# Optimization experiments

Measured on AMD Instinct MI355X. Metric: run time of the kernel, lower is better.

## Reference

```python
import jax, jax.numpy as jnp
import numpy as np

B, S, H, F, E, TOPK = 4, 2048, 1024, 3584, 8, 2
W_SCALE = 0.02  # keep router logits / activations numerically sane


def setup_inputs() -> dict:
    key = jax.random.key(0)
    k1, k2, k3, k4, k5 = jax.random.split(key, 5)
    return {
        "hidden_states": jax.random.normal(k1, (B, S, H), dtype=jnp.float32),
        "gate_w": jax.random.normal(k2, (E, H), dtype=jnp.float32) * W_SCALE,
        "w1": jax.random.normal(k3, (E, F, H), dtype=jnp.float32) * W_SCALE,
        "w2": jax.random.normal(k4, (E, H, F), dtype=jnp.float32) * W_SCALE,
        "w3": jax.random.normal(k5, (E, F, H), dtype=jnp.float32) * W_SCALE,
        "top_k": TOPK,
    }


def reference(hidden_states, gate_w, w1, w2, w3, top_k):
    b, s, h = hidden_states.shape
    x = hidden_states.reshape(-1, h)                       # [T, H]
    router_logits = x @ gate_w.T                           # [T, E]
    probs = jax.nn.softmax(router_logits.astype(jnp.float32), axis=-1)
    routing_weights, selected_experts = jax.lax.top_k(probs, top_k)  # [T, k]
    routing_weights = routing_weights / routing_weights.sum(axis=-1, keepdims=True)
    routing_weights = routing_weights.astype(x.dtype)
    n_experts = gate_w.shape[0]
    # combine weights: [T, E], zero for unselected experts
    combine = (jax.nn.one_hot(selected_experts, n_experts, dtype=routing_weights.dtype)
               * routing_weights[..., None]).sum(axis=1)
    out = jnp.zeros_like(x)
    for e in range(n_experts):
        hgate = jax.nn.silu(x @ w1[e].T) * (x @ w3[e].T)   # [T, F]
        out = out + (hgate @ w2[e].T) * combine[:, e:e + 1]
    return out.reshape(b, s, h), router_logits
```

## Files before the change

kernel.cpp:

```cpp
#include <hip/hip_runtime.h>
#include <hip/hip_bf16.h>
#include <stdint.h>

#define T_TOK 8192
#define H_DIM 1024
#define F_DIM 3584
#define E_NUM 8

#define BM 128
#define BN 128
#define BK 32
#define LDT 40

typedef __attribute__((ext_vector_type(8))) short bf16x8;
typedef __attribute__((ext_vector_type(4))) float f32x4;

__device__ __forceinline__ short f2bf(float f) {
    union { float f; uint32_t u; } v; v.f = f;
    uint32_t r = v.u + 0x7fffu + ((v.u >> 16) & 1u);
    return (short)(r >> 16);
}

__device__ __forceinline__ uint32_t pack_bf16x2(float a, float b) {
    union { float f; uint32_t u; } ua, ub;
    ua.f = a; ub.f = b;
    return __builtin_amdgcn_perm(ub.u + 0x8000u, ua.u + 0x8000u, 0x07060302u);
}

__device__ __forceinline__ void cvt_store16(const f32x4* v, short* dst) {
    uint32_t w[8];
    #pragma unroll
    for (int i = 0; i < 4; i++) {
        w[2*i]   = pack_bf16x2(v[i][0], v[i][1]);
        w[2*i+1] = pack_bf16x2(v[i][2], v[i][3]);
    }
    ((uint32_t*)dst)[0] = w[0]; ((uint32_t*)dst)[1] = w[1];
    ((uint32_t*)dst)[2] = w[2]; ((uint32_t*)dst)[3] = w[3];
    ((uint32_t*)dst)[4] = w[4]; ((uint32_t*)dst)[5] = w[5];
    ((uint32_t*)dst)[6] = w[6]; ((uint32_t*)dst)[7] = w[7];
}

__device__ __forceinline__ void zero16_store(short* dst) {
    bf16x8 z;
    #pragma unroll
    for (int i = 0; i < 8; i++) z[i] = 0;
    *(bf16x8*)dst = z;
    *((bf16x8*)dst + 1) = z;
}

__device__ __forceinline__ void load16(f32x4* dst, const float* __restrict__ src) {
    const f32x4* p = (const f32x4*)src;
    #pragma unroll
    for (int i = 0; i < 4; i++) dst[i] = p[i];
}

__global__ void router_kernel(const float* __restrict__ x,
                              const float* __restrict__ gate_w,
                              float* __restrict__ logits_out,
                              int* __restrict__ counts,
                              int* __restrict__ lists,
                              float* __restrict__ wgt) {
    int wave = (blockIdx.x * blockDim.x + threadIdx.x) >> 6;
    int lane = threadIdx.x & 63;
    if (wave >= T_TOK) return;
    const float* xr = x + (size_t)wave * H_DIM;

    float acc[E_NUM];
    #pragma unroll
    for (int e = 0; e < E_NUM; e++) acc[e] = 0.f;

    for (int i = lane; i < H_DIM; i += 64) {
        float xv = xr[i];
        #pragma unroll
        for (int e = 0; e < E_NUM; e++) acc[e] += xv * gate_w[e * H_DIM + i];
    }
    #pragma unroll
    for (int off = 32; off > 0; off >>= 1) {
        #pragma unroll
        for (int e = 0; e < E_NUM; e++) acc[e] += __shfl_xor(acc[e], off);
    }

    if (lane == 0) {
        int t = wave;
        #pragma unroll
        for (int e = 0; e < E_NUM; e++) logits_out[t * E_NUM + e] = acc[e];
        int i0 = 0; float v0 = acc[0];
        #pragma unroll
        for (int e = 1; e < E_NUM; e++) if (acc[e] > v0) { v0 = acc[e]; i0 = e; }
        int i1 = -1; float v1 = -1e30f;
        #pragma unroll
        for (int e = 0; e < E_NUM; e++) if (e != i0 && acc[e] > v1) { v1 = acc[e]; i1 = e; }
        float e1 = __expf(v1 - v0);
        float inv = 1.f / (1.f + e1);
        int a0 = 2 * t, a1 = 2 * t + 1;
        wgt[a0] = inv;
        wgt[a1] = e1 * inv;
        int p0 = atomicAdd(&counts[i0], 1);
        lists[i0 * T_TOK + p0] = a0;
        int p1 = atomicAdd(&counts[i1], 1);
        lists[i1 * T_TOK + p1] = a1;
    }
}

__global__ __launch_bounds__(256, 2)
void gemm1_kernel(const float* __restrict__ x,
                  const float* __restrict__ w1,
                  const float* __restrict__ w3,
                  const int* __restrict__ counts,
                  const int* __restrict__ lists,
                  unsigned short* __restrict__ hgate) {
    const int e = blockIdx.z;
    const int count = counts[e];
    const int mbase = blockIdx.y * BM;
    if (mbase >= count) return;
    const int nbase = blockIdx.x * BN;

    __shared__ short As[BM * LDT];
    __shared__ short B1s[BN * LDT];
    __shared__ short B3s[BN * LDT];

    const int tid = threadIdx.x;
    const int r = tid >> 1;
    const int half = tid & 1;

    const float* arow = nullptr;
    {
        int m = mbase + r;
        if (m < count) {
            int a = lists[e * T_TOK + m];
            arow = x + (size_t)(a >> 1) * H_DIM;
        }
    }
    const float* b1row = w1 + ((size_t)e * F_DIM + (nbase + r)) * H_DIM;
    const float* b3row = w3 + ((size_t)e * F_DIM + (nbase + r)) * H_DIM;

    const int lane = tid & 63;
    const int wid = tid >> 6;
    const int wm = wid >> 1, wn = wid & 1;
    const int lr = lane & 15, lq = lane >> 4;

    f32x4 acc1[4][4], acc3[4][4];
    #pragma unroll
    for (int i = 0; i < 4; i++)
        #pragma unroll
        for (int j = 0; j < 4; j++) {
            acc1[i][j] = (f32x4){0.f, 0.f, 0.f, 0.f};
            acc3[i][j] = (f32x4){0.f, 0.f, 0.f, 0.f};
        }

    f32x4 ap[4], b1p[4], b3p[4];
    {
        const int koff = half * 16;
        if (arow) load16(ap, arow + koff);
        load16(b1p, b1row + koff);
        load16(b3p, b3row + koff);
    }

    short* adst  = &As[r * LDT + half * 16];
    short* b1dst = &B1s[r * LDT + half * 16];
    short* b3dst = &B3s[r * LDT + half * 16];

    for (int k0 = 0; k0 < H_DIM; k0 += BK) {
        if (arow) cvt_store16(ap, adst); else zero16_store(adst);
        cvt_store16(b1p, b1dst);
        cvt_store16(b3p, b3dst);
        __syncthreads();

        int kn = k0 + BK;
        if (kn < H_DIM) {
            const int koff = kn + half * 16;
            if (arow) load16(ap, arow + koff);
            load16(b1p, b1row + koff);
            load16(b3p, b3row + koff);
        }

        bf16x8 af[4], b1f[4], b3f[4];
        #pragma unroll
        for (int i = 0; i < 4; i++)
            af[i] = *(const bf16x8*)&As[(wm * 64 + i * 16 + lr) * LDT + lq * 8];
        #pragma unroll
        for (int j = 0; j < 4; j++) {
            b1f[j] = *(const bf16x8*)&B1s[(wn * 64 + j * 16 + lr) * LDT + lq * 8];
            b3f[j] = *(const bf16x8*)&B3s[(wn * 64 + j * 16 + lr) * LDT + lq * 8];
        }
        #pragma unroll
        for (int i = 0; i < 4; i++)
            #pragma unroll
            for (int j = 0; j < 4; j++) {
                acc1[i][j] = __builtin_amdgcn_mfma_f32_16x16x32_bf16(af[i], b1f[j], acc1[i][j], 0, 0, 0);
                acc3[i][j] = __builtin_amdgcn_mfma_f32_16x16x32_bf16(af[i], b3f[j], acc3[i][j], 0, 0, 0);
            }
        __syncthreads();
    }

    #pragma unroll
    for (int i = 0; i < 4; i++) {
        #pragma unroll
        for (int rg = 0; rg < 4; rg++) {
            int mm = mbase + wm * 64 + i * 16 + lq * 4 + rg;
            if (mm >= count) continue;
            int a = lists[e * T_TOK + mm];
            unsigned short* hrow = hgate + (size_t)a * F_DIM + nbase;
            #pragma unroll
            for (int j = 0; j < 4; j++) {
                float g = acc1[i][j][rg];
                float u = acc3[i][j][rg];
                float s = (g / (1.f + __expf(-g))) * u;
                hrow[wn * 64 + j * 16 + lr] = (unsigned short)f2bf(s);
            }
        }
    }
}

__global__ __launch_bounds__(256, 2)
void gemm2_kernel(const unsigned short* __restrict__ hgate,
                  const float* __restrict__ w2,
                  const int* __restrict__ counts,
                  const int* __restrict__ lists,
                  const float* __restrict__ wgt,
                  float* __restrict__ out) {
    const int e = blockIdx.z;
    const int count = counts[e];
    const int mbase = blockIdx.y * BM;
    if (mbase >= count) return;
    const int nbase = blockIdx.x * BN;

    __shared__ short As[BM * LDT];
    __shared__ short Bs[BN * LDT];

    const int tid = threadIdx.x;
    const int r = tid >> 1;
    const int half = tid & 1;

    const unsigned short* arow = nullptr;
    {
        int m = mbase + r;
        if (m < count) {
            int a = lists[e * T_TOK + m];
            arow = hgate + (size_t)a * F_DIM;
        }
    }
    const float* brow = w2 + ((size_t)e * H_DIM + (nbase + r)) * F_DIM;

    const int lane = tid & 63;
    const int wid = tid >> 6;
    const int wm = wid >> 1, wn = wid & 1;
    const int lr = lane & 15, lq = lane >> 4;

    f32x4 acc[4][4];
    #pragma unroll
    for (int i = 0; i < 4; i++)
        #pragma unroll
        for (int j = 0; j < 4; j++) acc[i][j] = (f32x4){0.f, 0.f, 0.f, 0.f};

    bf16x8 a2p[2];
    f32x4 bp[4];
    {
        const int koff = half * 16;
        if (arow) {
            const bf16x8* p = (const bf16x8*)(arow + koff);
            a2p[0] = p[0]; a2p[1] = p[1];
        }
        load16(bp, brow + koff);
    }

    short* adst = &As[r * LDT + half * 16];
    short* bdst = &Bs[r * LDT + half * 16];

    for (int k0 = 0; k0 < F_DIM; k0 += BK) {
        if (arow) {
            *(bf16x8*)adst = a2p[0];
            *((bf16x8*)adst + 1) = a2p[1];
        } else {
            zero16_store(adst);
        }
        cvt_store16(bp, bdst);
        __syncthreads();

        int kn = k0 + BK;
        if (kn < F_DIM) {
            const int koff = kn + half * 16;
            if (arow) {
                const bf16x8* p = (const bf16x8*)(arow + koff);
                a2p[0] = p[0]; a2p[1] = p[1];
            }
            load16(bp, brow + koff);
        }

        bf16x8 af[4], bf[4];
        #pragma unroll
        for (int i = 0; i < 4; i++)
            af[i] = *(const bf16x8*)&As[(wm * 64 + i * 16 + lr) * LDT + lq * 8];
        #pragma unroll
        for (int j = 0; j < 4; j++)
            bf[j] = *(const bf16x8*)&Bs[(wn * 64 + j * 16 + lr) * LDT + lq * 8];
        #pragma unroll
        for (int i = 0; i < 4; i++)
            #pragma unroll
            for (int j = 0; j < 4; j++)
                acc[i][j] = __builtin_amdgcn_mfma_f32_16x16x32_bf16(af[i], bf[j], acc[i][j], 0, 0, 0);
        __syncthreads();
    }

    #pragma unroll
    for (int i = 0; i < 4; i++) {
        #pragma unroll
        for (int rg = 0; rg < 4; rg++) {
            int mm = mbase + wm * 64 + i * 16 + lq * 4 + rg;
            if (mm >= count) continue;
            int a = lists[e * T_TOK + mm];
            float w = wgt[a];
            int t = a >> 1;
            float* orow = out + (size_t)t * H_DIM + nbase;
            #pragma unroll
            for (int j = 0; j < 4; j++)
                atomicAdd(&orow[wn * 64 + j * 16 + lr], acc[i][j][rg] * w);
        }
    }
}

extern "C" void kernel_launch(void* const* d_in, const int* in_sizes, int n_in,
                              void* d_out, int out_size, void* d_ws, size_t ws_size,
                              hipStream_t stream) {
    const float* x      = (const float*)d_in[0];
    const float* gate_w = (const float*)d_in[1];
    const float* w1     = (const float*)d_in[2];
    const float* w2     = (const float*)d_in[3];
    const float* w3     = (const float*)d_in[4];

    float* out    = (float*)d_out;
    float* logits = out + (size_t)T_TOK * H_DIM;

    char* ws = (char*)d_ws;
    int*   counts = (int*)(ws + 0);
    int*   lists  = (int*)(ws + 1024);
    float* wgt    = (float*)(ws + 1024 + (size_t)E_NUM * T_TOK * 4);
    unsigned short* hgate =
        (unsigned short*)(ws + 1024 + (size_t)E_NUM * T_TOK * 4 + (size_t)T_TOK * 2 * 4);

    hipMemsetAsync(counts, 0, E_NUM * sizeof(int), stream);
    hipMemsetAsync(out, 0, (size_t)T_TOK * H_DIM * sizeof(float), stream);

    router_kernel<<<T_TOK / 4, 256, 0, stream>>>(x, gate_w, logits, counts, lists, wgt);

    gemm1_kernel<<<dim3(F_DIM / BN, T_TOK / BM, E_NUM), 256, 0, stream>>>(
        x, w1, w3, counts, lists, hgate);

    gemm2_kernel<<<dim3(H_DIM / BN, T_TOK / BM, E_NUM), 256, 0, stream>>>(
        hgate, w2, counts, lists, wgt, out);
}
```

Measured before the change: 1.227 ms.

## Pre-convert inputs to bf16 and stage GEMM tiles with direct global-to-LDS loads

```diff
diff --git a/kernel.cpp b/kernel.cpp
--- a/kernel.cpp
+++ b/kernel.cpp
@@ -14,6 +14,7 @@
 
 typedef __attribute__((ext_vector_type(8))) short bf16x8;
 typedef __attribute__((ext_vector_type(4))) float f32x4;
+typedef __attribute__((ext_vector_type(4))) unsigned int u32x4;
 
 __device__ __forceinline__ short f2bf(float f) {
     union { float f; uint32_t u; } v; v.f = f;
@@ -34,10 +35,8 @@
         w[2*i]   = pack_bf16x2(v[i][0], v[i][1]);
         w[2*i+1] = pack_bf16x2(v[i][2], v[i][3]);
     }
-    ((uint32_t*)dst)[0] = w[0]; ((uint32_t*)dst)[1] = w[1];
-    ((uint32_t*)dst)[2] = w[2]; ((uint32_t*)dst)[3] = w[3];
-    ((uint32_t*)dst)[4] = w[4]; ((uint32_t*)dst)[5] = w[5];
-    ((uint32_t*)dst)[6] = w[6]; ((uint32_t*)dst)[7] = w[7];
+    #pragma unroll
+    for (int i = 0; i < 8; i++) ((uint32_t*)dst)[i] = w[i];
 }
 
 __device__ __forceinline__ void zero16_store(short* dst) {
@@ -52,6 +51,13 @@
     const f32x4* p = (const f32x4*)src;
     #pragma unroll
     for (int i = 0; i < 4; i++) dst[i] = p[i];
+}
+
+__device__ __forceinline__ void gload16(const unsigned short* g, unsigned short* l) {
+    __builtin_amdgcn_global_load_lds(
+        (const __attribute__((address_space(1))) void*)g,
+        (__attribute__((address_space(3))) void*)l,
+        16, 0, 0);
 }
 
 __global__ void router_kernel(const float* __restrict__ x,
@@ -102,13 +108,218 @@
     }
 }
 
+__global__ void cvt_bf16_kernel(const float* __restrict__ in,
+                                unsigned short* __restrict__ out, int n8) {
+    int i = blockIdx.x * blockDim.x + threadIdx.x;
+    int stride = gridDim.x * blockDim.x;
+    for (; i < n8; i += stride) {
+        const f32x4* p = (const f32x4*)in + 2 * (size_t)i;
+        f32x4 v0 = p[0], v1 = p[1];
+        u32x4 w;
+        w[0] = pack_bf16x2(v0[0], v0[1]);
+        w[1] = pack_bf16x2(v0[2], v0[3]);
+        w[2] = pack_bf16x2(v1[0], v1[1]);
+        w[3] = pack_bf16x2(v1[2], v1[3]);
+        *(u32x4*)(out + 8 * (size_t)i) = w;
+    }
+}
+
 __global__ __launch_bounds__(256, 2)
-void gemm1_kernel(const float* __restrict__ x,
-                  const float* __restrict__ w1,
-                  const float* __restrict__ w3,
-                  const int* __restrict__ counts,
-                  const int* __restrict__ lists,
-                  unsigned short* __restrict__ hgate) {
+void gemm1_bf(const unsigned short* __restrict__ xbf,
+              const unsigned short* __restrict__ w1bf,
+              const unsigned short* __restrict__ w3bf,
+              const int* __restrict__ counts,
+              const int* __restrict__ lists,
+              const unsigned short* __restrict__ zbuf,
+              unsigned short* __restrict__ hgate) {
+    const int e = blockIdx.z;
+    const int count = counts[e];
+    const int mbase = blockIdx.x * BM;
+    if (mbase >= count) return;
+    const int nbase = blockIdx.y * BN;
+
+    __shared__ unsigned short As[BM * BK];
+    __shared__ unsigned short B1s[BN * BK];
+    __shared__ unsigned short B3s[BN * BK];
+
+    const int tid = threadIdx.x;
+    const int lane = tid & 63;
+    const int w = tid >> 6;
+    const int sr0 = w * 16 + (lane >> 2);
+    const int sr1 = 64 + sr0;
+    const int chunk = lane & 3;
+
+    const unsigned short* a0;
+    const unsigned short* a1;
+    {
+        int m = mbase + sr0;
+        a0 = (m < count) ? xbf + (size_t)(lists[e * T_TOK + m] >> 1) * H_DIM + chunk * 8
+                         : zbuf + chunk * 8;
+        m = mbase + sr1;
+        a1 = (m < count) ? xbf + (size_t)(lists[e * T_TOK + m] >> 1) * H_DIM + chunk * 8
+                         : zbuf + chunk * 8;
+    }
+    const unsigned short* b10 = w1bf + ((size_t)e * F_DIM + nbase + sr0) * H_DIM + chunk * 8;
+    const unsigned short* b11 = w1bf + ((size_t)e * F_DIM + nbase + sr1) * H_DIM + chunk * 8;
+    const unsigned short* b30 = w3bf + ((size_t)e * F_DIM + nbase + sr0) * H_DIM + chunk * 8;
+    const unsigned short* b31 = w3bf + ((size_t)e * F_DIM + nbase + sr1) * H_DIM + chunk * 8;
+
+    unsigned short* Al0  = &As[(size_t)(w * 16) * BK];
+    unsigned short* Al1  = &As[(size_t)(64 + w * 16) * BK];
+    unsigned short* B1l0 = &B1s[(size_t)(w * 16) * BK];
+    unsigned short* B1l1 = &B1s[(size_t)(64 + w * 16) * BK];
+    unsigned short* B3l0 = &B3s[(size_t)(w * 16) * BK];
+    unsigned short* B3l1 = &B3s[(size_t)(64 + w * 16) * BK];
+
+    const int wm = w >> 1, wn = w & 1;
+    const int lr = lane & 15, lq = lane >> 4;
+
+    f32x4 acc1[4][4], acc3[4][4];
+    #pragma unroll
+    for (int i = 0; i < 4; i++)
+        #pragma unroll
+        for (int j = 0; j < 4; j++) {
+            acc1[i][j] = (f32x4){0.f, 0.f, 0.f, 0.f};
+            acc3[i][j] = (f32x4){0.f, 0.f, 0.f, 0.f};
+        }
+
+    for (int k0 = 0; k0 < H_DIM; k0 += BK) {
+        gload16(a0, Al0);  gload16(a1, Al1);
+        gload16(b10, B1l0); gload16(b11, B1l1);
+        gload16(b30, B3l0); gload16(b31, B3l1);
+        a0 += BK; a1 += BK; b10 += BK; b11 += BK; b30 += BK; b31 += BK;
+        __syncthreads();
+
+        bf16x8 af[4];
+        #pragma unroll
+        for (int i = 0; i < 4; i++)
+            af[i] = *(const bf16x8*)&As[(wm * 64 + i * 16 + lr) * BK + lq * 8];
+        #pragma unroll
+        for (int j = 0; j < 4; j++) {
+            bf16x8 b1f = *(const bf16x8*)&B1s[(wn * 64 + j * 16 + lr) * BK + lq * 8];
+            bf16x8 b3f = *(const bf16x8*)&B3s[(wn * 64 + j * 16 + lr) * BK + lq * 8];
+            #pragma unroll
+            for (int i = 0; i < 4; i++) {
+                acc1[i][j] = __builtin_amdgcn_mfma_f32_16x16x32_bf16(af[i], b1f, acc1[i][j], 0, 0, 0);
+                acc3[i][j] = __builtin_amdgcn_mfma_f32_16x16x32_bf16(af[i], b3f, acc3[i][j], 0, 0, 0);
+            }
+        }
+        __syncthreads();
+    }
+
+    #pragma unroll
+    for (int i = 0; i < 4; i++) {
+        #pragma unroll
+        for (int rg = 0; rg < 4; rg++) {
+            int mm = mbase + wm * 64 + i * 16 + lq * 4 + rg;
+            if (mm >= count) continue;
+            int a = lists[e * T_TOK + mm];
+            unsigned short* hrow = hgate + (size_t)a * F_DIM + nbase;
+            #pragma unroll
+            for (int j = 0; j < 4; j++) {
+                float g = acc1[i][j][rg];
+                float u = acc3[i][j][rg];
+                float s = (g / (1.f + __expf(-g))) * u;
+                hrow[wn * 64 + j * 16 + lr] = (unsigned short)f2bf(s);
+            }
+        }
+    }
+}
+
+__global__ __launch_bounds__(256, 3)
+void gemm2_bf(const unsigned short* __restrict__ hgate,
+              const unsigned short* __restrict__ w2bf,
+              const int* __restrict__ counts,
+              const int* __restrict__ lists,
+              const float* __restrict__ wgt,
+              const unsigned short* __restrict__ zbuf,
+              float* __restrict__ out) {
+    const int e = blockIdx.z;
+    const int count = counts[e];
+    const int mbase = blockIdx.x * BM;
+    if (mbase >= count) return;
+    const int nbase = blockIdx.y * BN;
+
+    __shared__ unsigned short As[BM * BK];
+    __shared__ unsigned short Bs[BN * BK];
+
+    const int tid = threadIdx.x;
+    const int lane = tid & 63;
+    const int w = tid >> 6;
+    const int sr0 = w * 16 + (lane >> 2);
+    const int sr1 = 64 + sr0;
+    const int chunk = lane & 3;
+
+    const unsigned short* a0;
+    const unsigned short* a1;
+    {
+        int m = mbase + sr0;
+        a0 = (m < count) ? hgate + (size_t)lists[e * T_TOK + m] * F_DIM + chunk * 8
+                         : zbuf + chunk * 8;
+        m = mbase + sr1;
+        a1 = (m < count) ? hgate + (size_t)lists[e * T_TOK + m] * F_DIM + chunk * 8
+                         : zbuf + chunk * 8;
+    }
+    const unsigned short* b0 = w2bf + ((size_t)e * H_DIM + nbase + sr0) * F_DIM + chunk * 8;
+    const unsigned short* b1 = w2bf + ((size_t)e * H_DIM + nbase + sr1) * F_DIM + chunk * 8;
+
+    unsigned short* Al0 = &As[(size_t)(w * 16) * BK];
+    unsigned short* Al1 = &As[(size_t)(64 + w * 16) * BK];
+    unsigned short* Bl0 = &Bs[(size_t)(w * 16) * BK];
+    unsigned short* Bl1 = &Bs[(size_t)(64 + w * 16) * BK];
+
+    const int wm = w >> 1, wn = w & 1;
+    const int lr = lane & 15, lq = lane >> 4;
+
+    f32x4 acc[4][4];
+    #pragma unroll
+    for (int i = 0; i < 4; i++)
+        #pragma unroll
+        for (int j = 0; j < 4; j++) acc[i][j] = (f32x4){0.f, 0.f, 0.f, 0.f};
+
+    for (int k0 = 0; k0 < F_DIM; k0 += BK) {
+        gload16(a0, Al0); gload16(a1, Al1);
+        gload16(b0, Bl0); gload16(b1, Bl1);
+        a0 += BK; a1 += BK; b0 += BK; b1 += BK;
+        __syncthreads();
+
+        bf16x8 af[4];
+        #pragma unroll
+        for (int i = 0; i < 4; i++)
+            af[i] = *(const bf16x8*)&As[(wm * 64 + i * 16 + lr) * BK + lq * 8];
+        #pragma unroll
+        for (int j = 0; j < 4; j++) {
+            bf16x8 bf = *(const bf16x8*)&Bs[(wn * 64 + j * 16 + lr) * BK + lq * 8];
+            #pragma unroll
+            for (int i = 0; i < 4; i++)
+                acc[i][j] = __builtin_amdgcn_mfma_f32_16x16x32_bf16(af[i], bf, acc[i][j], 0, 0, 0);
+        }
+        __syncthreads();
+    }
+
+    #pragma unroll
+    for (int i = 0; i < 4; i++) {
+        #pragma unroll
+        for (int rg = 0; rg < 4; rg++) {
+            int mm = mbase + wm * 64 + i * 16 + lq * 4 + rg;
+            if (mm >= count) continue;
+            int a = lists[e * T_TOK + mm];
+            float wv = wgt[a];
+            float* orow = out + (size_t)(a >> 1) * H_DIM + nbase;
+            #pragma unroll
+            for (int j = 0; j < 4; j++)
+                atomicAdd(&orow[wn * 64 + j * 16 + lr], acc[i][j][rg] * wv);
+        }
+    }
+}
+
+__global__ __launch_bounds__(256, 2)
+void gemm1_f32(const float* __restrict__ x,
+               const float* __restrict__ w1,
+               const float* __restrict__ w3,
+               const int* __restrict__ counts,
+               const int* __restrict__ lists,
+               unsigned short* __restrict__ hgate) {
     const int e = blockIdx.z;
     const int count = counts[e];
     const int mbase = blockIdx.y * BM;
@@ -126,10 +337,7 @@
     const float* arow = nullptr;
     {
         int m = mbase + r;
-        if (m < count) {
-            int a = lists[e * T_TOK + m];
-            arow = x + (size_t)(a >> 1) * H_DIM;
-        }
+        if (m < count) arow = x + (size_t)(lists[e * T_TOK + m] >> 1) * H_DIM;
     }
     const float* b1row = w1 + ((size_t)e * F_DIM + (nbase + r)) * H_DIM;
     const float* b3row = w3 + ((size_t)e * F_DIM + (nbase + r)) * H_DIM;
@@ -155,7 +363,6 @@
         load16(b1p, b1row + koff);
         load16(b3p, b3row + koff);
     }
-
     short* adst  = &As[r * LDT + half * 16];
     short* b1dst = &B1s[r * LDT + half * 16];
     short* b3dst = &B3s[r * LDT + half * 16];
@@ -165,7 +372,6 @@
         cvt_store16(b1p, b1dst);
         cvt_store16(b3p, b3dst);
         __syncthreads();
-
         int kn = k0 + BK;
         if (kn < H_DIM) {
             const int koff = kn + half * 16;
@@ -173,26 +379,22 @@
             load16(b1p, b1row + koff);
             load16(b3p, b3row + koff);
         }
-
-        bf16x8 af[4], b1f[4], b3f[4];
+        bf16x8 af[4];
         #pragma unroll
         for (int i = 0; i < 4; i++)
             af[i] = *(const bf16x8*)&As[(wm * 64 + i * 16 + lr) * LDT + lq * 8];
         #pragma unroll
         for (int j = 0; j < 4; j++) {
-            b1f[j] = *(const bf16x8*)&B1s[(wn * 64 + j * 16 + lr) * LDT + lq * 8];
-            b3f[j] = *(const bf16x8*)&B3s[(wn * 64 + j * 16 + lr) * LDT + lq * 8];
-        }
-        #pragma unroll
-        for (int i = 0; i < 4; i++)
-            #pragma unroll
-            for (int j = 0; j < 4; j++) {
-                acc1[i][j] = __builtin_amdgcn_mfma_f32_16x16x32_bf16(af[i], b1f[j], acc1[i][j], 0, 0, 0);
-                acc3[i][j] = __builtin_amdgcn_mfma_f32_16x16x32_bf16(af[i], b3f[j], acc3[i][j], 0, 0, 0);
+            bf16x8 b1f = *(const bf16x8*)&B1s[(wn * 64 + j * 16 + lr) * LDT + lq * 8];
+            bf16x8 b3f = *(const bf16x8*)&B3s[(wn * 64 + j * 16 + lr) * LDT + lq * 8];
+            #pragma unroll
+            for (int i = 0; i < 4; i++) {
+                acc1[i][j] = __builtin_amdgcn_mfma_f32_16x16x32_bf16(af[i], b1f, acc1[i][j], 0, 0, 0);
+                acc3[i][j] = __builtin_amdgcn_mfma_f32_16x16x32_bf16(af[i], b3f, acc3[i][j], 0, 0, 0);
             }
-        __syncthreads();
-    }
-
+        }
+        __syncthreads();
+    }
     #pragma unroll
     for (int i = 0; i < 4; i++) {
         #pragma unroll
@@ -213,12 +415,12 @@
 }
 
 __global__ __launch_bounds__(256, 2)
-void gemm2_kernel(const unsigned short* __restrict__ hgate,
-                  const float* __restrict__ w2,
-                  const int* __restrict__ counts,
-                  const int* __restrict__ lists,
-                  const float* __restrict__ wgt,
-                  float* __restrict__ out) {
+void gemm2_f32(const unsigned short* __restrict__ hgate,
+               const float* __restrict__ w2,
+               const int* __restrict__ counts,
+               const int* __restrict__ lists,
+               const float* __restrict__ wgt,
+               float* __restrict__ out) {
     const int e = blockIdx.z;
     const int count = counts[e];
     const int mbase = blockIdx.y * BM;
@@ -235,10 +437,7 @@
     const unsigned short* arow = nullptr;
     {
         int m = mbase + r;
-        if (m < count) {
-            int a = lists[e * T_TOK + m];
-            arow = hgate + (size_t)a * F_DIM;
-        }
+        if (m < count) arow = hgate + (size_t)lists[e * T_TOK + m] * F_DIM;
     }
     const float* brow = w2 + ((size_t)e * H_DIM + (nbase + r)) * F_DIM;
 
@@ -263,7 +462,6 @@
         }
         load16(bp, brow + koff);
     }
-
     short* adst = &As[r * LDT + half * 16];
     short* bdst = &Bs[r * LDT + half * 16];
 
@@ -271,12 +469,9 @@
         if (arow) {
             *(bf16x8*)adst = a2p[0];
             *((bf16x8*)adst + 1) = a2p[1];
-        } else {
-            zero16_store(adst);
-        }
+        } else zero16_store(adst);
         cvt_store16(bp, bdst);
         __syncthreads();
-
         int kn = k0 + BK;
         if (kn < F_DIM) {
             const int koff = kn + half * 16;
@@ -286,22 +481,19 @@
             }
             load16(bp, brow + koff);
         }
-
-        bf16x8 af[4], bf[4];
+        bf16x8 af[4];
         #pragma unroll
         for (int i = 0; i < 4; i++)
             af[i] = *(const bf16x8*)&As[(wm * 64 + i * 16 + lr) * LDT + lq * 8];
         #pragma unroll
-        for (int j = 0; j < 4; j++)
-            bf[j] = *(const bf16x8*)&Bs[(wn * 64 + j * 16 + lr) * LDT + lq * 8];
-        #pragma unroll
-        for (int i = 0; i < 4; i++)
-            #pragma unroll
-            for (int j = 0; j < 4; j++)
-                acc[i][j] = __builtin_amdgcn_mfma_f32_16x16x32_bf16(af[i], bf[j], acc[i][j], 0, 0, 0);
-        __syncthreads();
-    }
-
+        for (int j = 0; j < 4; j++) {
+            bf16x8 bf = *(const bf16x8*)&Bs[(wn * 64 + j * 16 + lr) * LDT + lq * 8];
+            #pragma unroll
+            for (int i = 0; i < 4; i++)
+                acc[i][j] = __builtin_amdgcn_mfma_f32_16x16x32_bf16(af[i], bf, acc[i][j], 0, 0, 0);
+        }
+        __syncthreads();
+    }
     #pragma unroll
     for (int i = 0; i < 4; i++) {
         #pragma unroll
@@ -309,12 +501,11 @@
             int mm = mbase + wm * 64 + i * 16 + lq * 4 + rg;
             if (mm >= count) continue;
             int a = lists[e * T_TOK + mm];
-            float w = wgt[a];
-            int t = a >> 1;
-            float* orow = out + (size_t)t * H_DIM + nbase;
+            float wv = wgt[a];
+            float* orow = out + (size_t)(a >> 1) * H_DIM + nbase;
             #pragma unroll
             for (int j = 0; j < 4; j++)
-                atomicAdd(&orow[wn * 64 + j * 16 + lr], acc[i][j][rg] * w);
+                atomicAdd(&orow[wn * 64 + j * 16 + lr], acc[i][j][rg] * wv);
         }
     }
 }
@@ -331,21 +522,64 @@
     float* out    = (float*)d_out;
     float* logits = out + (size_t)T_TOK * H_DIM;
 
+    const size_t W_ELEMS = (size_t)E_NUM * F_DIM * H_DIM;
+    const size_t X_ELEMS = (size_t)T_TOK * H_DIM;
+
+    const size_t off_counts = 0;
+    const size_t off_zbuf   = 256;
+    const size_t off_lists  = 8704;
+    const size_t off_wgt    = off_lists + (size_t)E_NUM * T_TOK * 4;
+    const size_t off_xbf    = off_wgt + (size_t)T_TOK * 2 * 4;
+    const size_t off_w1bf   = off_xbf + X_ELEMS * 2;
+    const size_t off_w3bf   = off_w1bf + W_ELEMS * 2;
+    const size_t off_w2bf   = off_w3bf + W_ELEMS * 2;
+    const size_t off_hg     = off_w2bf + W_ELEMS * 2;
+    const size_t NEED       = off_hg + (size_t)T_TOK * 2 * F_DIM * 2;
+
     char* ws = (char*)d_ws;
-    int*   counts = (int*)(ws + 0);
-    int*   lists  = (int*)(ws + 1024);
-    float* wgt    = (float*)(ws + 1024 + (size_t)E_NUM * T_TOK * 4);
-    unsigned short* hgate =
-        (unsigned short*)(ws + 1024 + (size_t)E_NUM * T_TOK * 4 + (size_t)T_TOK * 2 * 4);
-
-    hipMemsetAsync(counts, 0, E_NUM * sizeof(int), stream);
-    hipMemsetAsync(out, 0, (size_t)T_TOK * H_DIM * sizeof(float), stream);
-
-    router_kernel<<<T_TOK / 4, 256, 0, stream>>>(x, gate_w, logits, counts, lists, wgt);
-
-    gemm1_kernel<<<dim3(F_DIM / BN, T_TOK / BM, E_NUM), 256, 0, stream>>>(
-        x, w1, w3, counts, lists, hgate);
-
-    gemm2_kernel<<<dim3(H_DIM / BN, T_TOK / BM, E_NUM), 256, 0, stream>>>(
-        hgate, w2, counts, lists, wgt, out);
-}
+
+    if (ws_size >= NEED) {
+        int*   counts = (int*)(ws + off_counts);
+        unsigned short* zbuf = (unsigned short*)(ws + off_zbuf);
+        int*   lists  = (int*)(ws + off_lists);
+        float* wgt    = (float*)(ws + off_wgt);
+        unsigned short* xbf  = (unsigned short*)(ws + off_xbf);
+        unsigned short* w1bf = (unsigned short*)(ws + off_w1bf);
+        unsigned short* w3bf = (unsigned short*)(ws + off_w3bf);
+        unsigned short* w2bf = (unsigned short*)(ws + off_w2bf);
+        unsigned short* hgate = (unsigned short*)(ws + off_hg);
+
+        hipMemsetAsync(ws, 0, 8704, stream);
+        hipMemsetAsync(out, 0, (size_t)T_TOK * H_DIM * sizeof(float), stream);
+
+        router_kernel<<<T_TOK / 4, 256, 0, stream>>>(x, gate_w, logits, counts, lists, wgt);
+
+        cvt_bf16_kernel<<<2048, 256, 0, stream>>>(x,  xbf,  (int)(X_ELEMS / 8));
+        cvt_bf16_kernel<<<4096, 256, 0, stream>>>(w1, w1bf, (int)(W_ELEMS / 8));
+        cvt_bf16_kernel<<<4096, 256, 0, stream>>>(w3, w3bf, (int)(W_ELEMS / 8));
+        cvt_bf16_kernel<<<4096, 256, 0, stream>>>(w2, w2bf, (int)(W_ELEMS / 8));
+
+        gemm1_bf<<<dim3(T_TOK / BM, F_DIM / BN, E_NUM), 256, 0, stream>>>(
+            xbf, w1bf, w3bf, counts, lists, zbuf, hgate);
+
+        gemm2_bf<<<dim3(T_TOK / BM, H_DIM / BN, E_NUM), 256, 0, stream>>>(
+            hgate, w2bf, counts, lists, wgt, zbuf, out);
+    } else {
+        int*   counts = (int*)(ws + 0);
+        int*   lists  = (int*)(ws + 1024);
+        float* wgt    = (float*)(ws + 1024 + (size_t)E_NUM * T_TOK * 4);
+        unsigned short* hgate =
+            (unsigned short*)(ws + 1024 + (size_t)E_NUM * T_TOK * 4 + (size_t)T_TOK * 2 * 4);
+
+        hipMemsetAsync(counts, 0, E_NUM * sizeof(int), stream);
+        hipMemsetAsync(out, 0, (size_t)T_TOK * H_DIM * sizeof(float), stream);
+
+        router_kernel<<<T_TOK / 4, 256, 0, stream>>>(x, gate_w, logits, counts, lists, wgt);
+
+        gemm1_f32<<<dim3(F_DIM / BN, T_TOK / BM, E_NUM), 256, 0, stream>>>(
+            x, w1, w3, counts, lists, hgate);
+
+        gemm2_f32<<<dim3(H_DIM / BN, T_TOK / BM, E_NUM), 256, 0, stream>>>(
+            hgate, w2, counts, lists, wgt, out);
+    }
+}
```

New measurement: 1.425 ms. 16.1% more time.
